# Performance work log

Measured on AMD Instinct MI355X. Metric: run time of the kernel, lower is better.

## Reference

```python
import jax, jax.numpy as jnp
import numpy as np

N = 1536
F = 64          # in_features
F_IN = F + 1    # include_adj adds adjacency channel
OUT = 64


def setup_inputs() -> dict:
    key = jax.random.key(0)
    k1, k2, k3, k4 = jax.random.split(key, 4)
    feat = jax.random.normal(k1, (N, F), dtype=jnp.float32)
    adj = jax.random.uniform(k2, (N, N), dtype=jnp.float32)
    # nn.Linear init: U(-1/sqrt(fan_in), 1/sqrt(fan_in))
    bound = 1.0 / np.sqrt(F_IN)
    W = jax.random.uniform(k3, (OUT, F_IN), minval=-bound, maxval=bound, dtype=jnp.float32)
    b = jax.random.uniform(k4, (OUT,), minval=-bound, maxval=bound, dtype=jnp.float32)
    return {"feat": feat, "adj": adj, "W": W, "b": b}


def reference(feat, adj, W, b):
    # pairwise abs-diff via broadcasting (no repeat): [N, N, F]
    feat_diff = jnp.abs(feat[None, :, :] - feat[:, None, :])
    # concat adjacency as extra channel -> [N, N, F+1], then flatten rows
    x = jnp.concatenate([feat_diff, adj[:, :, None]], axis=2).reshape(N * N, F_IN)
    # Linear: x @ W.T + b -> [N*N, OUT]
    return x @ W.T + b
```

## Files before the change

### kernel.cpp

```cpp
#include <hip/hip_runtime.h>
#include <hip/hip_bf16.h>

#define N_NODES 1536
#define NF 64
#define NOUT 64
#define FIN 65
#define TI 8

typedef __bf16 bf16x8 __attribute__((ext_vector_type(8)));
typedef float f32x4 __attribute__((ext_vector_type(4)));

__global__ __launch_bounds__(256, 2)
void edge_gcn_mfma(const float* __restrict__ feat,
                   const float* __restrict__ adj,
                   const float* __restrict__ W,
                   const float* __restrict__ b,
                   float* __restrict__ out)
{
    const int tid  = threadIdx.x;
    const int lane = tid & 63;
    const int wv   = tid >> 6;
    const int l15  = lane & 15;
    const int lg   = lane >> 4;

    const int i0 = blockIdx.y * TI;
    const int j0 = blockIdx.x * 128;
    const int jw = j0 + wv * 32;

    __shared__ float lds[8192];
    __shared__ float fslab[TI * NF];
    float* const lbase = lds + wv * 2048;

    if (tid < 128) {
        const int row = tid >> 4;
        const int col = (tid & 15) * 4;
        *reinterpret_cast<f32x4*>(&fslab[row * NF + col]) =
            *reinterpret_cast<const f32x4*>(&feat[(size_t)(i0 + row) * NF + col]);
    }

    float av_pre[TI][2];
#pragma unroll
    for (int ii = 0; ii < TI; ++ii)
#pragma unroll
        for (int n = 0; n < 2; ++n)
            av_pre[ii][n] =
                adj[(size_t)(i0 + ii) * N_NODES + jw + n * 16 + l15];

    bf16x8 afrag[2][4];
#pragma unroll
    for (int kk = 0; kk < 2; ++kk) {
#pragma unroll
        for (int mo = 0; mo < 4; ++mo) {
            const float* wp = W + (mo * 16 + l15) * FIN + kk * 32 + lg * 8;
#pragma unroll
            for (int e = 0; e < 8; ++e) afrag[kk][mo][e] = (__bf16)wp[e];
        }
    }

    float fjr[2][2][8];
#pragma unroll
    for (int n = 0; n < 2; ++n) {
        const float* fjrow = feat + (jw + n * 16 + l15) * NF;
#pragma unroll
        for (int kk = 0; kk < 2; ++kk)
#pragma unroll
            for (int e = 0; e < 8; ++e)
                fjr[n][kk][e] = fjrow[kk * 32 + lg * 8 + e];
    }

    float wl[4][4], bv[4][4];
#pragma unroll
    for (int mo = 0; mo < 4; ++mo) {
        const float* bp = b + mo * 16 + lg * 4;
#pragma unroll
        for (int r = 0; r < 4; ++r) {
            bv[mo][r] = bp[r];
            wl[mo][r] = W[(mo * 16 + lg * 4 + r) * FIN + NF];
        }
    }

    __syncthreads();

#pragma unroll
    for (int ii = 0; ii < TI; ++ii) {
        const int i = i0 + ii;

        float fi[2][8];
#pragma unroll
        for (int kk = 0; kk < 2; ++kk) {
            const float* fp = &fslab[ii * NF + kk * 32 + lg * 8];
#pragma unroll
            for (int e = 0; e < 8; ++e) fi[kk][e] = fp[e];
        }

        f32x4 acc[4][2];
#pragma unroll
        for (int mo = 0; mo < 4; ++mo)
#pragma unroll
            for (int n = 0; n < 2; ++n)
#pragma unroll
                for (int r = 0; r < 4; ++r)
                    acc[mo][n][r] = bv[mo][r];

#pragma unroll
        for (int n = 0; n < 2; ++n) {
#pragma unroll
            for (int kk = 0; kk < 2; ++kk) {
                bf16x8 bfrag;
#pragma unroll
                for (int e = 0; e < 8; ++e)
                    bfrag[e] = (__bf16)fabsf(fjr[n][kk][e] - fi[kk][e]);
#pragma unroll
                for (int mo = 0; mo < 4; ++mo)
                    acc[mo][n] = __builtin_amdgcn_mfma_f32_16x16x32_bf16(
                        afrag[kk][mo], bfrag, acc[mo][n], 0, 0, 0);
            }
        }

#pragma unroll
        for (int n = 0; n < 2; ++n) {
            const int jrow = n * 16 + l15;
            const float av = av_pre[ii][n];
#pragma unroll
            for (int mo = 0; mo < 4; ++mo) {
                f32x4 v;
#pragma unroll
                for (int r = 0; r < 4; ++r)
                    v[r] = acc[mo][n][r] + av * wl[mo][r];
                const int swz = (mo * 16 + lg * 4) ^ ((l15 & 7) << 2);
                *reinterpret_cast<f32x4*>(lbase + jrow * 64 + swz) = v;
            }
        }

#pragma unroll
        for (int t = 0; t < 8; ++t) {
            const int jr = t * 4 + lg;
            const int oo = l15 * 4;
            f32x4 v = *reinterpret_cast<const f32x4*>(
                lbase + jr * 64 + (oo ^ ((jr & 7) << 2)));
            float* op = out + ((size_t)i * N_NODES + jw + jr) * NOUT + oo;
            *reinterpret_cast<f32x4*>(op) = v;
        }
    }
}

extern "C" void kernel_launch(void* const* d_in, const int* in_sizes, int n_in,
                              void* d_out, int out_size, void* d_ws, size_t ws_size,
                              hipStream_t stream) {
    const float* feat = (const float*)d_in[0];
    const float* adj  = (const float*)d_in[1];
    const float* W    = (const float*)d_in[2];
    const float* b    = (const float*)d_in[3];
    float* out = (float*)d_out;

    dim3 grid(N_NODES / 128, N_NODES / TI);
    dim3 block(256);
    edge_gcn_mfma<<<grid, block, 0, stream>>>(feat, adj, W, b, out);
}
```

Measured before the change: 128.1 us.

## Move adjacency and bias epilogue after LDS transpose to cut register pressure

Adjacency values are now staged into a shared-memory slab, and the bias plus adjacency-weight term is applied after the LDS transpose, using per-lane weights for the output columns each lane writes. This replaces 32 bias/weight registers and 16 prefetched adjacency registers with 8. The ii loop is no longer unrolled, and launch bounds ask for 3 blocks per SM, both aiming at higher occupancy on a store-bound kernel. The cost is an extra LDS read per output vector and less instruction-level overlap across rows. LDS use per block rises slightly, which may limit occupancy.

```diff
diff --git a/kernel.cpp b/kernel.cpp
--- a/kernel.cpp
+++ b/kernel.cpp
@@ -10,7 +10,7 @@
 typedef __bf16 bf16x8 __attribute__((ext_vector_type(8)));
 typedef float f32x4 __attribute__((ext_vector_type(4)));
 
-__global__ __launch_bounds__(256, 2)
+__global__ __launch_bounds__(256, 3)
 void edge_gcn_mfma(const float* __restrict__ feat,
                    const float* __restrict__ adj,
                    const float* __restrict__ W,
@@ -29,6 +29,7 @@
 
     __shared__ float lds[8192];
     __shared__ float fslab[TI * NF];
+    __shared__ float aslab[TI * 128];
     float* const lbase = lds + wv * 2048;
 
     if (tid < 128) {
@@ -37,14 +38,13 @@
         *reinterpret_cast<f32x4*>(&fslab[row * NF + col]) =
             *reinterpret_cast<const f32x4*>(&feat[(size_t)(i0 + row) * NF + col]);
     }
-
-    float av_pre[TI][2];
-#pragma unroll
-    for (int ii = 0; ii < TI; ++ii)
-#pragma unroll
-        for (int n = 0; n < 2; ++n)
-            av_pre[ii][n] =
-                adj[(size_t)(i0 + ii) * N_NODES + jw + n * 16 + l15];
+    {
+        const int row = tid >> 5;
+        const int col = (tid & 31) * 4;
+        *reinterpret_cast<f32x4*>(&aslab[row * 128 + col]) =
+            *reinterpret_cast<const f32x4*>(
+                &adj[(size_t)(i0 + row) * N_NODES + j0 + col]);
+    }
 
     bf16x8 afrag[2][4];
 #pragma unroll
@@ -68,20 +68,16 @@
                 fjr[n][kk][e] = fjrow[kk * 32 + lg * 8 + e];
     }
 
-    float wl[4][4], bv[4][4];
+    float wlB[4], bvB[4];
 #pragma unroll
-    for (int mo = 0; mo < 4; ++mo) {
-        const float* bp = b + mo * 16 + lg * 4;
-#pragma unroll
-        for (int r = 0; r < 4; ++r) {
-            bv[mo][r] = bp[r];
-            wl[mo][r] = W[(mo * 16 + lg * 4 + r) * FIN + NF];
-        }
+    for (int r = 0; r < 4; ++r) {
+        wlB[r] = W[(l15 * 4 + r) * FIN + NF];
+        bvB[r] = b[l15 * 4 + r];
     }
 
     __syncthreads();
 
-#pragma unroll
+#pragma unroll 1
     for (int ii = 0; ii < TI; ++ii) {
         const int i = i0 + ii;
 
@@ -98,9 +94,7 @@
         for (int mo = 0; mo < 4; ++mo)
 #pragma unroll
             for (int n = 0; n < 2; ++n)
-#pragma unroll
-                for (int r = 0; r < 4; ++r)
-                    acc[mo][n][r] = bv[mo][r];
+                acc[mo][n] = (f32x4){0.f, 0.f, 0.f, 0.f};
 
 #pragma unroll
         for (int n = 0; n < 2; ++n) {
@@ -120,15 +114,10 @@
 #pragma unroll
         for (int n = 0; n < 2; ++n) {
             const int jrow = n * 16 + l15;
-            const float av = av_pre[ii][n];
 #pragma unroll
             for (int mo = 0; mo < 4; ++mo) {
-                f32x4 v;
-#pragma unroll
-                for (int r = 0; r < 4; ++r)
-                    v[r] = acc[mo][n][r] + av * wl[mo][r];
                 const int swz = (mo * 16 + lg * 4) ^ ((l15 & 7) << 2);
-                *reinterpret_cast<f32x4*>(lbase + jrow * 64 + swz) = v;
+                *reinterpret_cast<f32x4*>(lbase + jrow * 64 + swz) = acc[mo][n];
             }
         }
 
@@ -138,6 +127,10 @@
             const int oo = l15 * 4;
             f32x4 v = *reinterpret_cast<const f32x4*>(
                 lbase + jr * 64 + (oo ^ ((jr & 7) << 2)));
+            const float av = aslab[ii * 128 + wv * 32 + jr];
+#pragma unroll
+            for (int r = 0; r < 4; ++r)
+                v[r] = v[r] + av * wlB[r] + bvB[r];
             float* op = out + ((size_t)i * N_NODES + jw + jr) * NOUT + oo;
             *reinterpret_cast<f32x4*>(op) = v;
         }
```

After: 125.1 us. -2.3%, faster.
